# Kernel optimization log

Hardware: AMD Instinct MI355X
Metric: run time of the kernel (lower is better)

The kernel has to match this reference:

```python
import jax, jax.numpy as jnp
import numpy as np
from jax import lax

SCALES = [0.5, 0.25, 0.125, 0.0625]
D_MODEL = 256
IN_CH = 1


def setup_inputs() -> dict:
    key = jax.random.key(0)
    ks = jax.random.split(key, 16)
    x = jax.random.normal(ks[0], (2, D_MODEL, 256, 256), dtype=jnp.float32)
    m = jax.random.uniform(ks[1], (2, IN_CH, 256, 256), dtype=jnp.float32)
    s = 0.05
    Wq = jax.random.normal(ks[2], (D_MODEL, D_MODEL, 1, 1), jnp.float32) * s
    bq = jax.random.normal(ks[3], (D_MODEL,), jnp.float32) * s
    Wk = jax.random.normal(ks[4], (D_MODEL, D_MODEL, 1, 1), jnp.float32) * s
    bk = jax.random.normal(ks[5], (D_MODEL,), jnp.float32) * s
    Wv = jax.random.normal(ks[6], (D_MODEL, D_MODEL, 1, 1), jnp.float32) * s
    bv = jax.random.normal(ks[7], (D_MODEL,), jnp.float32) * s
    Wmq = jax.random.normal(ks[8], (D_MODEL, IN_CH, 1, 1), jnp.float32) * s
    bmq = jax.random.normal(ks[9], (D_MODEL,), jnp.float32) * s
    Wmk = jax.random.normal(ks[10], (D_MODEL, IN_CH, 1, 1), jnp.float32) * s
    bmk = jax.random.normal(ks[11], (D_MODEL,), jnp.float32) * s
    Wo = jax.random.normal(ks[12], (D_MODEL, D_MODEL, 3, 3), jnp.float32) * s
    bo = jax.random.normal(ks[13], (D_MODEL,), jnp.float32) * s
    return {"x": x, "m": m, "Wq": Wq, "bq": bq, "Wk": Wk, "bk": bk,
            "Wv": Wv, "bv": bv, "Wmq": Wmq, "bmq": bmq, "Wmk": Wmk, "bmk": bmk,
            "Wo": Wo, "bo": bo, "b": 1, "c": 256}


def _conv1x1(z, W, bias):
    # W: (O, I, 1, 1)
    return jnp.einsum('bihw,oi->bohw', z, W[:, :, 0, 0]) + bias[None, :, None, None]


def _forward(x, m, Wq, bq, Wk, bk, Wv, bv, Wmq, bmq, Wmk, bmk, Wo, bo, b, c):
    bt, _, h, w = x.shape  # h, w are multiples of 64 -> pad is zero
    t = bt // b
    n_scales = len(SCALES)
    d_k = c // n_scales

    q = _conv1x1(x, Wq, bq)
    k = _conv1x1(x, Wk, bk)
    v = _conv1x1(x, Wv, bv)
    mq = _conv1x1(m, Wmq, bmq)
    mk = _conv1x1(m, Wmk, bmk)

    outs = []
    for i, scale in enumerate(SCALES):
        height, width = int(h * scale), int(w * scale)
        out_h, out_w = h // height, w // width
        sl = slice(i * d_k, (i + 1) * d_k)

        def patch(z):
            # (b, t, d_k, out_h, height, out_w, width) -> (b, t*out_h*out_w, d_k*height*width)
            z = z[:, sl].reshape(b, t, d_k, out_h, height, out_w, width)
            z = z.transpose(0, 1, 3, 5, 2, 4, 6)
            return z.reshape(b, t * out_h * out_w, d_k * height * width)

        Q, K, V = patch(q), patch(k), patch(v)
        MQ, MK = patch(mq), patch(mk)
        inv_sqrt_d = 1.0 / jnp.sqrt(jnp.asarray(Q.shape[-1], jnp.float32))
        scores = jnp.einsum('bnd,bmd->bnm', Q, K) * inv_sqrt_d
        mask_scores = jnp.einsum('bnd,bmd->bnm', MQ, MK) * inv_sqrt_d
        p_attn = jax.nn.softmax(scores * mask_scores, axis=-1)
        y = jnp.einsum('bnm,bmd->bnd', p_attn, V)
        # back to (bt, d_k, h, w)
        y = y.reshape(b, t, out_h, out_w, d_k, height, width)
        y = y.transpose(0, 1, 4, 2, 5, 3, 6).reshape(bt, d_k, h, w)
        outs.append(y)

    out = jnp.concatenate(outs, axis=1)
    z = lax.conv_general_dilated(out, Wo, window_strides=(1, 1),
                                 padding=((1, 1), (1, 1)),
                                 dimension_numbers=('NCHW', 'OIHW', 'NCHW'))
    z = z + bo[None, :, None, None]
    return jnp.where(z > 0, z, 0.2 * z)  # LeakyReLU(0.2)


def reference(x, m, Wq, bq, Wk, bk, Wv, bv, Wmq, bmq, Wmk, bmk, Wo, bo, b, c):
    return _forward(x, m, Wq, bq, Wk, bk, Wv, bv, Wmq, bmq, Wmk, bmk, Wo, bo, b, c)
```

## Files before the change

kernel.cpp:

```cpp
#include <hip/hip_runtime.h>
#include <stdint.h>


typedef __attribute__((ext_vector_type(8))) short short8;
typedef __attribute__((ext_vector_type(4))) float floatx4;
typedef __attribute__((ext_vector_type(4))) unsigned int uintx4;

#define DEV static __device__ __forceinline__

DEV unsigned short f2bf(float f) {
  unsigned u = __builtin_bit_cast(unsigned, f);
  unsigned r = u + 0x7FFFu + ((u >> 16) & 1u);
  return (unsigned short)(r >> 16);
}

DEV void patch_row(int n, int sc, int lw, int& pt, int& sp0) {
  pt = n >> (2 + 2 * sc);
  int rem = n & ((4 << (2 * sc)) - 1);
  int oh = rem >> (1 + sc), ow = rem & ((2 << sc) - 1);
  sp0 = (oh << (lw + 8)) + (ow << lw);
}

__global__ void k_prep(const float* __restrict__ Wq, const float* __restrict__ Wk,
                       const float* __restrict__ Wv, const float* __restrict__ bq,
                       const float* __restrict__ bk, const float* __restrict__ bv,
                       const float* __restrict__ Wmq, const float* __restrict__ bmq,
                       const float* __restrict__ Wmk, const float* __restrict__ bmk,
                       const float* __restrict__ Wo, const float* __restrict__ bo,
                       unsigned short* __restrict__ wqkv, float* __restrict__ bias,
                       float* __restrict__ msc, unsigned short* __restrict__ wobf,
                       float* __restrict__ scoresG, unsigned int* __restrict__ pbuf) {
  int bid = blockIdx.x;
  int t = threadIdx.x;
  if (bid < 768) {
    const float* src = bid < 256 ? (Wq + bid * 256) : (bid < 512 ? (Wk + (bid - 256) * 256)
                                                                 : (Wv + (bid - 512) * 256));
    wqkv[bid * 256 + t] = f2bf(src[t]);
    if (t == 0) bias[bid] = bid < 256 ? bq[bid] : (bid < 512 ? bk[bid - 256] : bv[bid - 512]);
    return;
  }
  if (bid == 768) {
    int sc = t >> 6, lane = t & 63;
    int ch = sc * 64 + lane;
    float a0 = Wmq[ch] * Wmk[ch];
    float a1 = Wmq[ch] * bmk[ch];
    float a2 = bmq[ch] * Wmk[ch];
    float a3 = bmq[ch] * bmk[ch];
    for (int off = 32; off; off >>= 1) {
      a0 += __shfl_xor(a0, off); a1 += __shfl_xor(a1, off);
      a2 += __shfl_xor(a2, off); a3 += __shfl_xor(a3, off);
    }
    if (lane == 0) {
      msc[sc * 4 + 0] = a0; msc[sc * 4 + 1] = a1;
      msc[sc * 4 + 2] = a2; msc[sc * 4 + 3] = a3;
    }
    return;
  }
  int blk = bid - 769;
  if (blk < 2304) {
    int didx = blk >> 8, o = blk & 255, c = t;
    wobf[didx * 65536 + o * 256 + c] = f2bf(Wo[o * 2304 + c * 9 + didx]);
  } else {
    int i = (blk - 2304) * 256 + t;
    if (i < 559232) scoresG[i] = 0.f;
    if (i < 140032) pbuf[i] = 0u;
  }
}

__global__ __launch_bounds__(256) void k_xt(const float* __restrict__ x,
                                            unsigned short* __restrict__ xt) {
  __shared__ __align__(16) unsigned short tile[64][72];
  int p0 = blockIdx.x * 64, c0 = blockIdx.y * 64, t = blockIdx.z;
  int tid = threadIdx.x;
  {
    int cc = tid >> 2, pq = (tid & 3) * 16;
    const float* src = x + ((t * 256 + c0 + cc) * 65536 + p0 + pq);
    __align__(16) unsigned short tmp[16];
#pragma unroll
    for (int e = 0; e < 16; e += 4) {
      floatx4 v = *(const floatx4*)(src + e);
      tmp[e + 0] = f2bf(v[0]); tmp[e + 1] = f2bf(v[1]);
      tmp[e + 2] = f2bf(v[2]); tmp[e + 3] = f2bf(v[3]);
    }
    *(uintx4*)&tile[cc][pq] = *(const uintx4*)&tmp[0];
    *(uintx4*)&tile[cc][pq + 8] = *(const uintx4*)&tmp[8];
  }
  __syncthreads();
  {
    int pp = tid >> 2, cg = (tid & 3) * 16;
    __align__(16) unsigned short outv[16];
#pragma unroll
    for (int e = 0; e < 16; ++e) outv[e] = tile[cg + e][pp];
    unsigned short* dst = xt + ((t * 65536 + p0 + pp) * 256 + c0 + cg);
    *(uintx4*)dst = *(const uintx4*)&outv[0];
    *(uintx4*)(dst + 8) = *(const uintx4*)&outv[8];
  }
}

__global__ __launch_bounds__(256) void k_yt(const unsigned short* __restrict__ ynat,
                                            unsigned short* __restrict__ yt) {
  __shared__ __align__(16) unsigned short tile[64][72];
  int p0 = blockIdx.x * 64, c0 = blockIdx.y * 64, t = blockIdx.z;
  int tid = threadIdx.x;
  {
    int cc = tid >> 2, pq = (tid & 3) * 16;
    const unsigned short* src = ynat + ((t * 256 + c0 + cc) * 65536 + p0 + pq);
    *(uintx4*)&tile[cc][pq] = *(const uintx4*)src;
    *(uintx4*)&tile[cc][pq + 8] = *(const uintx4*)(src + 8);
  }
  __syncthreads();
  {
    int pp = tid >> 2, cg = (tid & 3) * 16;
    __align__(16) unsigned short outv[16];
#pragma unroll
    for (int e = 0; e < 16; ++e) outv[e] = tile[cg + e][pp];
    unsigned short* dst = yt + ((t * 65536 + p0 + pp) * 256 + c0 + cg);
    *(uintx4*)dst = *(const uintx4*)&outv[0];
    *(uintx4*)(dst + 8) = *(const uintx4*)&outv[8];
  }
}

__global__ __launch_bounds__(256, 2) void k_qkv(const unsigned short* __restrict__ xt,
                                                const unsigned short* __restrict__ wqkv,
                                                const float* __restrict__ bias,
                                                unsigned short* __restrict__ qkv) {
  extern __shared__ __align__(16) char smem[];
  auto As = (unsigned short (*)[64])(smem);
  auto Bs = (unsigned short (*)[64])(smem + 16384);
  auto Cs = (unsigned short (*)[280])(smem);
  int flat = blockIdx.x;
  int lg = (flat & 7) * 384 + (flat >> 3);
  int n_t = lg / 6, m_t = lg - n_t * 6;
  int n0 = n_t << 8, m0 = m_t << 7;
  int tid = threadIdx.x;
  int w = tid >> 6, l = tid & 63;
  int wr = w >> 1, wc = w & 1;
  int l15 = l & 15, lhi = l >> 4;
  int sr = tid >> 1, sbase = (tid & 1) * 4, r7 = sr & 7;
  int b7 = tid & 7;
  const unsigned short* gA = wqkv + (m0 + sr) * 256 + sbase * 8;
  const unsigned short* gB = xt + (n0 + tid) * 256;
  floatx4 zf = {0.f, 0.f, 0.f, 0.f};
  floatx4 acc[4][8];
#pragma unroll
  for (int i = 0; i < 4; ++i)
#pragma unroll
    for (int j = 0; j < 8; ++j) acc[i][j] = zf;
  uintx4 ra[4], rb[8];
#define QLOAD(K0) { const uintx4* pa = (const uintx4*)(gA + (K0)); \
                    ra[0] = pa[0]; ra[1] = pa[1]; ra[2] = pa[2]; ra[3] = pa[3]; \
                    const uintx4* pb = (const uintx4*)(gB + (K0)); \
                    rb[0] = pb[0]; rb[1] = pb[1]; rb[2] = pb[2]; rb[3] = pb[3]; \
                    rb[4] = pb[4]; rb[5] = pb[5]; rb[6] = pb[6]; rb[7] = pb[7]; }
  QLOAD(0);
#pragma unroll
  for (int ch = 0; ch < 4; ++ch) {
    __syncthreads();
#pragma unroll
    for (int j = 0; j < 4; ++j)
      *(uintx4*)&As[sr][((sbase + j) ^ r7) * 8] = ra[j];
#pragma unroll
    for (int j = 0; j < 8; ++j)
      *(uintx4*)&Bs[tid][(j ^ b7) * 8] = rb[j];
    __syncthreads();
    if (ch < 3) QLOAD((ch + 1) * 64);
#pragma unroll
    for (int kk = 0; kk < 2; ++kk) {
      short8 af[4];
#pragma unroll
      for (int f = 0; f < 4; ++f) {
        int arow = wr * 64 + f * 16 + l15;
        af[f] = *(const short8*)&As[arow][(((kk << 2) + lhi) ^ (arow & 7)) * 8];
      }
#pragma unroll
      for (int fn = 0; fn < 8; ++fn) {
        int brow = wc * 128 + fn * 16 + l15;
        short8 b = *(const short8*)&Bs[brow][(((kk << 2) + lhi) ^ (brow & 7)) * 8];
#pragma unroll
        for (int fm = 0; fm < 4; ++fm)
          acc[fm][fn] = __builtin_amdgcn_mfma_f32_16x16x32_bf16(af[fm], b, acc[fm][fn], 0, 0, 0);
      }
    }
  }
#undef QLOAD
#pragma unroll
  for (int h = 0; h < 2; ++h) {
    __syncthreads();
    if (wr == h) {
#pragma unroll
      for (int fm = 0; fm < 4; ++fm) {
#pragma unroll
        for (int rr = 0; rr < 4; ++rr) {
          int rl = fm * 16 + lhi * 4 + rr;
          float bv = bias[m0 + h * 64 + rl];
#pragma unroll
          for (int fn = 0; fn < 8; ++fn)
            Cs[rl][wc * 128 + fn * 16 + l15] = f2bf(acc[fm][fn][rr] + bv);
        }
      }
    }
    __syncthreads();
    {
      int p8 = (tid & 31) * 8;
      int pcol = n0 + p8;
      int t = pcol >> 16, p = pcol & 65535;
#pragma unroll
      for (int pass = 0; pass < 8; ++pass) {
        int rl = (tid >> 5) + pass * 8;
        uintx4 v = *(const uintx4*)&Cs[rl][p8];
        *(uintx4*)&qkv[((t * 768 + m0 + h * 64 + rl) << 16) + p] = v;
      }
    }
  }
}

__global__ __launch_bounds__(256) void k_mask(const float* __restrict__ m,
                                              float* __restrict__ G,
                                              float* __restrict__ rbuf) {
  int bid = blockIdx.x;
  int tid = threadIdx.x;
  if (bid >= 328) {
    int row = (bid - 328) * 4 + (tid >> 6);
    int lane = tid & 63;
    if (row < 680) {
      int sc, n;
      if (row < 8)        { sc = 0; n = row; }
      else if (row < 40)  { sc = 1; n = row - 8; }
      else if (row < 168) { sc = 2; n = row - 40; }
      else                { sc = 3; n = row - 168; }
      int lw = 7 - sc, W = 1 << lw;
      int pt, sp0;
      patch_row(n, sc, lw, pt, sp0);
      int base = pt * 65536 + sp0;
      int S = 1 << (14 - 2 * sc);
      float acc = 0.f;
      for (int s = lane; s < S; s += 64) {
        int hh = s >> lw, ww = s & (W - 1);
        acc += m[base + (hh << 8) + ww];
      }
      for (int off = 32; off; off >>= 1) acc += __shfl_xor(acc, off);
      if (lane == 0) rbuf[row] = acc;
    }
    return;
  }
  __shared__ __align__(16) float Ns[32][68];
  __shared__ __align__(16) float Ms[32][68];
  int sc, tn, tm, z, nchunks, soff;
  if (bid < 32)      { sc = 0; tn = 0; tm = 0; z = bid;      nchunks = 8; soff = 0; }
  else if (bid < 40) { sc = 1; tn = 0; tm = 0; z = bid - 32; nchunks = 8; soff = 64; }
  else if (bid < 72) { int r = bid - 40; int tl = r >> 1; sc = 2; tn = tl >> 2; tm = tl & 3; z = r & 1; nchunks = 8; soff = 1088; }
  else               { int tl = bid - 72; sc = 3; tn = tl >> 4; tm = tl & 15; z = 0; nchunks = 4; soff = 17472; }
  int lw = 7 - sc, W = 1 << lw, N = 8 << (2 * sc);
  int kbase = z * nchunks * 64;
  int n0 = tn * 32, m0 = tm * 32;
  bool isA = tid < 128;
  int u = tid & 127;
  int srow = u >> 2, sslot0 = (u & 3) * 4;
  int grow = (isA ? n0 : m0) + srow;
  bool valid = grow < N;
  int pt = 0, sp0 = 0;
  if (valid) patch_row(grow, sc, lw, pt, sp0);
  int gbase = pt * 65536 + sp0;
  int trc = tid >> 4, tcc = tid & 15;
  float a00 = 0.f, a01 = 0.f, a10 = 0.f, a11 = 0.f;
  floatx4 zf = {0.f, 0.f, 0.f, 0.f};
  for (int c = 0; c < nchunks; ++c) {
    int k0 = kbase + c * 64;
    floatx4 v[4];
#pragma unroll
    for (int j = 0; j < 4; ++j) {
      v[j] = zf;
      if (valid) {
        int s = k0 + (sslot0 + j) * 4;
        int hh = s >> lw, ww = s & (W - 1);
        v[j] = *(const floatx4*)(m + gbase + (hh << 8) + ww);
      }
    }
    __syncthreads();
    float* dstrow = isA ? &Ns[srow][0] : &Ms[srow][0];
#pragma unroll
    for (int j = 0; j < 4; ++j) *(floatx4*)&dstrow[(sslot0 + j) * 4] = v[j];
    __syncthreads();
#pragma unroll 4
    for (int k = 0; k < 64; k += 4) {
      floatx4 na = *(const floatx4*)&Ns[2 * trc][k];
      floatx4 nb = *(const floatx4*)&Ns[2 * trc + 1][k];
      floatx4 ma = *(const floatx4*)&Ms[2 * tcc][k];
      floatx4 mb = *(const floatx4*)&Ms[2 * tcc + 1][k];
#pragma unroll
      for (int e = 0; e < 4; ++e) {
        a00 += na[e] * ma[e]; a01 += na[e] * mb[e];
        a10 += nb[e] * ma[e]; a11 += nb[e] * mb[e];
      }
    }
  }
  int rn = n0 + 2 * trc, rm = m0 + 2 * tcc;
  float res[2][2] = {{a00, a01}, {a10, a11}};
#pragma unroll
  for (int i = 0; i < 2; ++i)
#pragma unroll
    for (int j = 0; j < 2; ++j) {
      if (rn + i < N && rm + j < N) {
        float* dst = &G[soff + (rn + i) * N + rm + j];
        if (sc < 3) atomicAdd(dst, res[i][j]); else *dst = res[i][j];
      }
    }
}

__global__ __launch_bounds__(256) void k_scores_all(const unsigned short* __restrict__ qkv,
                                                    float* __restrict__ scores) {
  __shared__ __align__(16) char sbuf[32768];
  int bid = blockIdx.x;
  int tid = threadIdx.x;
  int w = tid >> 6, l = tid & 63;
  int wr = w >> 1, wc = w & 1, l15 = l & 15, lhi = l >> 4;
  uintx4 zu = {0u, 0u, 0u, 0u};
  floatx4 zf = {0.f, 0.f, 0.f, 0.f};
  if (bid < 160) {
    auto As = (unsigned short (*)[64])(sbuf);
    auto Bs = (unsigned short (*)[64])(sbuf + 16384);
    int lg = (bid & 7) * 20 + (bid >> 3);
    int sc, tn, tm, z, soff;
    if (lg < 32) { sc = 2; tn = 0; tm = 0; z = lg; soff = 1088; }
    else { int r = lg - 32; int tl = r >> 3; sc = 3; tn = tl >> 2; tm = tl & 3; z = r & 7; soff = 17472; }
    int N = 8 << (2 * sc);
    int lw = 7 - sc, W = 1 << lw, lS = 14 - 2 * sc;
    int n0 = tn * 128, m0 = tm * 128;
    int kbase = z * 2048;
    int sr = tid >> 1, sbase = (tid & 1) * 4, r7 = sr & 7;
    int ptA, spA, ptB, spB;
    patch_row(n0 + sr, sc, lw, ptA, spA);
    patch_row(m0 + sr, sc, lw, ptB, spB);
    int baseA = (ptA * 768 + sc * 64) * 65536 + spA;
    int baseB = (ptB * 768 + 256 + sc * 64) * 65536 + spB;
    floatx4 acc[4][4];
#pragma unroll
    for (int i = 0; i < 4; ++i)
#pragma unroll
      for (int j = 0; j < 4; ++j) acc[i][j] = zf;
    uintx4 ra[4], rb[4];
#define GLOAD(K0) { \
  _Pragma("unroll") for (int j = 0; j < 4; ++j) { \
    int k = kbase + (K0) + (sbase + j) * 8; \
    int cl = k >> lS; int s = k & ((1 << lS) - 1); \
    int hh = s >> lw, ww = s & (W - 1); \
    int off = cl * 65536 + (hh << 8) + ww; \
    ra[j] = *(const uintx4*)(qkv + baseA + off); \
    rb[j] = *(const uintx4*)(qkv + baseB + off); } }
    GLOAD(0);
    for (int st = 0; st < 32; ++st) {
      __syncthreads();
#pragma unroll
      for (int j = 0; j < 4; ++j) {
        *(uintx4*)&As[sr][((sbase + j) ^ r7) * 8] = ra[j];
        *(uintx4*)&Bs[sr][((sbase + j) ^ r7) * 8] = rb[j];
      }
      __syncthreads();
      if (st < 31) GLOAD((st + 1) * 64);
#pragma unroll
      for (int kk = 0; kk < 2; ++kk) {
        short8 af[4], bfr[4];
#pragma unroll
        for (int f = 0; f < 4; ++f) {
          int arow = wr * 64 + f * 16 + l15;
          af[f] = *(const short8*)&As[arow][(((kk << 2) + lhi) ^ (arow & 7)) * 8];
          int brow = wc * 64 + f * 16 + l15;
          bfr[f] = *(const short8*)&Bs[brow][(((kk << 2) + lhi) ^ (brow & 7)) * 8];
        }
#pragma unroll
        for (int fm = 0; fm < 4; ++fm)
#pragma unroll
          for (int fn = 0; fn < 4; ++fn)
            acc[fm][fn] = __builtin_amdgcn_mfma_f32_16x16x32_bf16(af[fm], bfr[fn], acc[fm][fn], 0, 0, 0);
      }
    }
#undef GLOAD
#pragma unroll
    for (int fm = 0; fm < 4; ++fm) {
      int nrow = n0 + wr * 64 + fm * 16 + lhi * 4;
#pragma unroll
      for (int rr = 0; rr < 4; ++rr) {
#pragma unroll
        for (int fn = 0; fn < 4; ++fn) {
          int mcol = m0 + wc * 64 + fn * 16 + l15;
          atomicAdd(&scores[soff + (nrow + rr) * N + mcol], acc[fm][fn][rr]);
        }
      }
    }
    return;
  }
  {
    auto As = (unsigned short (*)[136])(sbuf);
    auto Bs = (unsigned short (*)[136])(sbuf + 8704);
    int b2 = bid - 160;
    int sc, z, soff;
    if (b2 < 256) { sc = 0; z = b2;       soff = 0; }
    else          { sc = 1; z = b2 - 256; soff = 64; }
    int lw = 7 - sc, W = 1 << lw, lS = 14 - 2 * sc, N = 8 << (2 * sc);
    int kbase = z * 4096;
    floatx4 acc = zf;
    bool isA = tid < 128;
    int u = tid & 127;
    int srow = u >> 2, sslot0 = (u & 3) * 4;
    int grow = srow;
    int cb = (isA ? 0 : 256) + sc * 64;
    int pt = 0, sp0 = 0;
    bool valid = grow < N;
    if (valid) patch_row(grow, sc, lw, pt, sp0);
    int rowbase = (pt * 768 + cb) * 65536 + sp0;
    uintx4 r[4];
#define SLOAD(KS) { int kb2 = kbase + (KS) * 128; \
  _Pragma("unroll") for (int j = 0; j < 4; ++j) { \
    uintx4 v = zu; \
    if (valid) { int k = kb2 + (sslot0 + j) * 8; \
      int cl = k >> lS; int s = k & ((1 << lS) - 1); \
      int hh = s >> lw, ww = s & (W - 1); \
      v = *(const uintx4*)(qkv + rowbase + cl * 65536 + (hh << 8) + ww); } \
    r[j] = v; } }
    SLOAD(0);
    for (int ks = 0; ks < 32; ++ks) {
      __syncthreads();
      {
        unsigned short* dstrow = isA ? &As[srow][0] : &Bs[srow][0];
#pragma unroll
        for (int j = 0; j < 4; ++j) *(uintx4*)&dstrow[(sslot0 + j) * 8] = r[j];
      }
      __syncthreads();
      if (ks < 31) SLOAD(ks + 1);
#pragma unroll
      for (int kk = 0; kk < 4; ++kk) {
        short8 a = *(const short8*)&As[wr * 16 + l15][(kk * 4 + lhi) * 8];
        short8 b = *(const short8*)&Bs[wc * 16 + l15][(kk * 4 + lhi) * 8];
        acc = __builtin_amdgcn_mfma_f32_16x16x32_bf16(a, b, acc, 0, 0, 0);
      }
    }
#undef SLOAD
    int rrow = wr * 16 + lhi * 4;
    int ccol = wc * 16 + l15;
    if (ccol < N) {
#pragma unroll
      for (int rr = 0; rr < 4; ++rr)
        if (rrow + rr < N) atomicAdd(&scores[soff + (rrow + rr) * N + ccol], acc[rr]);
    }
  }
}

__global__ void k_softmax(const float* __restrict__ scores, const float* __restrict__ G,
                          const float* __restrict__ rbuf, const float* __restrict__ msc,
                          unsigned short* __restrict__ pbuf) {
  int row = blockIdx.x, lane = threadIdx.x;
  int sc, n, roff, soff, poff;
  if (row < 8)        { sc = 0; n = row;       roff = 0;   soff = 0;     poff = 0; }
  else if (row < 40)  { sc = 1; n = row - 8;   roff = 8;   soff = 64;    poff = 512; }
  else if (row < 168) { sc = 2; n = row - 40;  roff = 40;  soff = 1088;  poff = 1536; }
  else                { sc = 3; n = row - 168; roff = 168; soff = 17472; poff = 17920; }
  int N = 8 << (2 * sc);
  int Kpad = (sc < 2) ? 32 : N;
  float Sf = (float)(1 << (14 - 2 * sc));
  float invD = 1.0f / (float)(1 << (20 - 2 * sc));
  float alpha = msc[sc * 4 + 0], beta = msc[sc * 4 + 1];
  float gamma = msc[sc * 4 + 2], delta = msc[sc * 4 + 3];
  float rn = rbuf[roff + n];
  float vals[8];
  float mx = -1e30f;
#pragma unroll
  for (int j = 0; j < 8; ++j) {
    float v = -1e30f;
    int mcol = lane + j * 64;
    if (j * 64 < N && mcol < N) {
      float sq = scores[soff + n * N + mcol];
      float g = G[soff + n * N + mcol];
      float rm = rbuf[roff + mcol];
      v = sq * (alpha * g + beta * rn + gamma * rm + delta * Sf) * invD;
    }
    vals[j] = v;
    mx = fmaxf(mx, v);
  }
  for (int off = 32; off; off >>= 1) mx = fmaxf(mx, __shfl_xor(mx, off));
  float sum = 0.f;
#pragma unroll
  for (int j = 0; j < 8; ++j) {
    int mcol = lane + j * 64;
    float e = 0.f;
    if (j * 64 < N && mcol < N) e = __expf(vals[j] - mx);
    vals[j] = e;
    sum += e;
  }
  for (int off = 32; off; off >>= 1) sum += __shfl_xor(sum, off);
  float inv = 1.f / sum;
#pragma unroll
  for (int j = 0; j < 8; ++j) {
    int mcol = lane + j * 64;
    if (j * 64 < N && mcol < N) pbuf[poff + n * Kpad + mcol] = f2bf(vals[j] * inv);
  }
}

__global__ __launch_bounds__(256) void k_pv(const unsigned short* __restrict__ qkv,
                                            const unsigned short* __restrict__ pbuf,
                                            unsigned short* __restrict__ ynat) {
  int bid = blockIdx.x;
  int sc, bx, by;
  if (bid < 4096)      { sc = 0; bx = bid; by = 0; }
  else if (bid < 6144) { sc = 1; bx = bid - 4096; by = 0; }
  else if (bid < 8192) { int r = bid - 6144; sc = 2; bx = r >> 1; by = r & 1; }
  else                 { int r = bid - 8192; sc = 3; bx = r >> 3; by = r & 7; }
  int WR    = (sc == 0) ? 1 : (sc == 1) ? 2 : 4;
  int logWC = (sc == 0) ? 2 : (sc == 1) ? 1 : 0;
  int poff  = (sc == 0) ? 0 : (sc == 1) ? 512 : (sc == 2) ? 1536 : 17920;
  int lw = 7 - sc, W = 1 << lw;
  int lS = 14 - 2 * sc;
  int N = 8 << (2 * sc);
  int Kpad = (sc < 2) ? 32 : N;
  int WC = 1 << logWC;
  int d0 = bx * (WC * 64);
  int nb = by * (WR * 16);
  __shared__ __align__(16) unsigned short As[2][64][40];
  __shared__ __align__(16) unsigned short Bt[2][256][32];
  int tid = threadIdx.x;
  int w = tid >> 6, l = tid & 63;
  int wr = w >> logWC, wc = w & (WC - 1);
  int l15 = l & 15, lhi = l >> 4;
  floatx4 zf = {0.f, 0.f, 0.f, 0.f};
  floatx4 acc[4];
#pragma unroll
  for (int i = 0; i < 4; ++i) acc[i] = zf;
  int bmp = tid & 15;
  int dg = tid >> 4;
  bool act0 = (WC > 1) || (dg < 8);
  bool has1 = (WC == 4);
  bool doA = tid < WR * 64;
  int arow = tid >> 2, akg = (tid & 3) * 8;
  int ksteps = Kpad >> 5;
  uintx4 zu = {0u, 0u, 0u, 0u};
  int vcb = (512 + sc * 64) * 65536;
  uintx4 av = zu, lo0 = zu, hi0 = zu, lo1 = zu, hi1 = zu;
#define PLOADS(KS) { int k0 = (KS) * 32; \
    av = zu; lo0 = zu; hi0 = zu; lo1 = zu; hi1 = zu; \
    if (doA) av = *(const uintx4*)(pbuf + poff + (nb + arow) * Kpad + k0 + akg); \
    int gm0 = k0 + 2 * bmp, gm1 = gm0 + 1; \
    bool mv0 = gm0 < N, mv1 = gm1 < N; \
    int pt0 = 0, sp00 = 0, pt1 = 0, sp01 = 0; \
    if (mv0) patch_row(gm0, sc, lw, pt0, sp00); \
    if (mv1) patch_row(gm1, sc, lw, pt1, sp01); \
    { int d = d0 + dg * 8; int cl = d >> lS; int s = d & ((1 << lS) - 1); \
      int hh = s >> lw, ww = s & (W - 1); int sp = (hh << 8) + ww; \
      if (act0 && mv0) lo0 = *(const uintx4*)(qkv + pt0 * 768 * 65536 + vcb + cl * 65536 + sp00 + sp); \
      if (act0 && mv1) hi0 = *(const uintx4*)(qkv + pt1 * 768 * 65536 + vcb + cl * 65536 + sp01 + sp); } \
    if (has1) { int d = d0 + (dg + 16) * 8; int cl = d >> lS; int s = d & ((1 << lS) - 1); \
      int hh = s >> lw, ww = s & (W - 1); int sp = (hh << 8) + ww; \
      if (mv0) lo1 = *(const uintx4*)(qkv + pt0 * 768 * 65536 + vcb + cl * 65536 + sp00 + sp); \
      if (mv1) hi1 = *(const uintx4*)(qkv + pt1 * 768 * 65536 + vcb + cl * 65536 + sp01 + sp); } }
  PLOADS(0);
  for (int ks = 0; ks < ksteps; ++ks) {
    int b = ks & 1;
    if (doA) *(uintx4*)&As[b][arow][akg] = av;
    if (act0) {
      int du = dg * 8;
#pragma unroll
      for (int j = 0; j < 8; ++j) {
        int d = du + j;
        unsigned losh = (lo0[j >> 1] >> ((j & 1) * 16)) & 0xFFFFu;
        unsigned hish = (hi0[j >> 1] >> ((j & 1) * 16)) & 0xFFFFu;
        unsigned wv = losh | (hish << 16);
        int slot = (bmp >> 2) ^ ((d >> 1) & 3) ^ ((d >> 3) & 3);
        ((unsigned int*)&Bt[b][d][0])[slot * 4 + (bmp & 3)] = wv;
      }
    }
    if (has1) {
      int du = (dg + 16) * 8;
#pragma unroll
      for (int j = 0; j < 8; ++j) {
        int d = du + j;
        unsigned losh = (lo1[j >> 1] >> ((j & 1) * 16)) & 0xFFFFu;
        unsigned hish = (hi1[j >> 1] >> ((j & 1) * 16)) & 0xFFFFu;
        unsigned wv = losh | (hish << 16);
        int slot = (bmp >> 2) ^ ((d >> 1) & 3) ^ ((d >> 3) & 3);
        ((unsigned int*)&Bt[b][d][0])[slot * 4 + (bmp & 3)] = wv;
      }
    }
    __syncthreads();
    if (ks + 1 < ksteps) PLOADS(ks + 1);
    short8 a = *(const short8*)&As[b][wr * 16 + l15][lhi * 8];
#pragma unroll
    for (int fn = 0; fn < 4; ++fn) {
      int row = wc * 64 + fn * 16 + l15;
      int slot = lhi ^ ((row >> 1) & 3) ^ ((row >> 3) & 3);
      short8 bb = *(const short8*)&Bt[b][row][slot * 8];
      acc[fn] = __builtin_amdgcn_mfma_f32_16x16x32_bf16(a, bb, acc[fn], 0, 0, 0);
    }
  }
#undef PLOADS
  int nrow = nb + wr * 16 + lhi * 4;
#pragma unroll
  for (int rr = 0; rr < 4; ++rr) {
    int n = nrow + rr;
    if (n < N) {
      int pt, sp0;
      patch_row(n, sc, lw, pt, sp0);
#pragma unroll
      for (int fn = 0; fn < 4; ++fn) {
        int d = d0 + wc * 64 + fn * 16 + l15;
        int cl = d >> lS;
        int s = d & ((1 << lS) - 1);
        int hh = s >> lw, ww = s & (W - 1);
        int c = sc * 64 + cl;
        ynat[(pt * 256 + c) * 65536 + sp0 + (hh << 8) + ww] = f2bf(acc[fn][rr]);
      }
    }
  }
}

__global__ __launch_bounds__(256, 3) void k_conv(const unsigned short* __restrict__ yt,
                                                 const unsigned short* __restrict__ wo,
                                                 const float* __restrict__ bo,
                                                 float* __restrict__ out) {
  __shared__ __align__(16) unsigned short As[64][128];
  __shared__ __align__(16) unsigned short Bs[130][64];
  int flat = blockIdx.x;
  int lg = ((flat & 7) << 8) + (flat >> 3);
  int n_t = lg >> 2, m_t = lg & 3;
  int n0 = n_t << 8, m0 = m_t << 6;
  int tt = n0 >> 16, yy = (n0 >> 8) & 255;
  int tid = threadIdx.x;
  int w = tid >> 6, l = tid & 63;
  int l15 = l & 15, lhi = l >> 4;
  bool doA = tid < 192;
  int a_dx = tid >> 6, a_o = tid & 63;
  bool doBh = tid >= 254;
  floatx4 zf = {0.f, 0.f, 0.f, 0.f};
  floatx4 acc[4][4];
#pragma unroll
  for (int i = 0; i < 4; ++i)
#pragma unroll
    for (int j = 0; j < 4; ++j) acc[i][j] = zf;
  uintx4 zu = {0u, 0u, 0u, 0u};
  uintx4 rb[4], ra[4], rh[4];
  const unsigned short* ybase = yt + (tt << 24);
#define CLOAD(ST) { \
    int dy = (ST) >> 3, cc = ((ST) & 7) << 5; \
    int yq = yy + dy - 1; \
    bool yv = (unsigned)yq < 256u; \
    { int xq = tid - 1; \
      if (yv && (unsigned)xq < 256u) { \
        const uintx4* p = (const uintx4*)(ybase + ((yq << 8) + xq) * 256 + cc); \
        rb[0] = p[0]; rb[1] = p[1]; rb[2] = p[2]; rb[3] = p[3]; \
      } else { rb[0] = zu; rb[1] = zu; rb[2] = zu; rb[3] = zu; } } \
    if (doA) { \
      const uintx4* p = (const uintx4*)(wo + (dy * 3 + a_dx) * 65536 + (m0 + a_o) * 256 + cc); \
      ra[0] = p[0]; ra[1] = p[1]; ra[2] = p[2]; ra[3] = p[3]; \
    } else if (doBh) { \
      int xq = tid + 1;   \
      if (yv && xq < 256) { \
        const uintx4* p = (const uintx4*)(ybase + ((yq << 8) + xq) * 256 + cc); \
        rh[0] = p[0]; rh[1] = p[1]; rh[2] = p[2]; rh[3] = p[3]; \
      } else { rh[0] = zu; rh[1] = zu; rh[2] = zu; rh[3] = zu; } } }
  CLOAD(0);
  for (int st = 0; st < 24; ++st) {
    __syncthreads();
    {
      int brow = tid >> 1, bhf = (tid & 1) * 4, br7 = brow & 7;
#pragma unroll
      for (int j = 0; j < 4; ++j)
        *(uintx4*)&Bs[brow][((bhf + j) ^ br7) * 8] = rb[j];
      if (doA) {
        int o7 = a_o & 7;
#pragma unroll
        for (int j = 0; j < 4; ++j)
          *(uintx4*)&As[a_o][((a_dx * 4 + j) ^ o7) * 8] = ra[j];
      } else if (doBh) {
        int xh = tid + 2;
        int brow2 = xh >> 1, bhf2 = (xh & 1) * 4, br72 = brow2 & 7;
#pragma unroll
        for (int j = 0; j < 4; ++j)
          *(uintx4*)&Bs[brow2][((bhf2 + j) ^ br72) * 8] = rh[j];
      }
    }
    __syncthreads();
    if (st < 23) CLOAD(st + 1);
#pragma unroll
    for (int dx = 0; dx < 3; ++dx) {
      short8 af[4];
#pragma unroll
      for (int f = 0; f < 4; ++f) {
        int ol = f * 16 + l15;
        af[f] = *(const short8*)&As[ol][((dx * 4 + lhi) ^ (ol & 7)) * 8];
      }
#pragma unroll
      for (int fn = 0; fn < 4; ++fn) {
        int xh = w * 64 + fn * 16 + l15 + dx;
        short8 b = *(const short8*)&Bs[xh >> 1][((((xh & 1) * 4 + lhi)) ^ ((xh >> 1) & 7)) * 8];
#pragma unroll
        for (int fm = 0; fm < 4; ++fm)
          acc[fm][fn] = __builtin_amdgcn_mfma_f32_16x16x32_bf16(af[fm], b, acc[fm][fn], 0, 0, 0);
      }
    }
  }
#undef CLOAD
#pragma unroll
  for (int fm = 0; fm < 4; ++fm) {
    int o = m0 + fm * 16 + lhi * 4;
#pragma unroll
    for (int rr = 0; rr < 4; ++rr) {
      float bias = bo[o + rr];
#pragma unroll
      for (int fn = 0; fn < 4; ++fn) {
        int xcol = w * 64 + fn * 16 + l15;
        float z = acc[fm][fn][rr] + bias;
        out[((tt * 256 + o + rr) << 16) + (yy << 8) + xcol] = z > 0.f ? z : 0.2f * z;
      }
    }
  }
}

extern "C" void kernel_launch(void* const* d_in, const int* in_sizes, int n_in,
                              void* d_out, int out_size, void* d_ws, size_t ws_size,
                              hipStream_t stream) {
  const float* x   = (const float*)d_in[0];
  const float* m   = (const float*)d_in[1];
  const float* Wq  = (const float*)d_in[2];
  const float* bq  = (const float*)d_in[3];
  const float* Wk  = (const float*)d_in[4];
  const float* bk  = (const float*)d_in[5];
  const float* Wv  = (const float*)d_in[6];
  const float* bv  = (const float*)d_in[7];
  const float* Wmq = (const float*)d_in[8];
  const float* bmq = (const float*)d_in[9];
  const float* Wmk = (const float*)d_in[10];
  const float* bmk = (const float*)d_in[11];
  const float* Wo  = (const float*)d_in[12];
  const float* bo  = (const float*)d_in[13];

  char* ws = (char*)d_ws;
  unsigned short* qkv   = (unsigned short*)(ws);
  unsigned short* xtb   = (unsigned short*)(ws + 201326592);
  unsigned short* wqkv  = (unsigned short*)(ws + 268435456);
  unsigned short* wobf  = (unsigned short*)(ws + 268828672);
  float* bias           = (float*)(ws + 270008320);
  float* msc            = (float*)(ws + 270011392);
  float* scores         = (float*)(ws + 270011456);
  float* G              = (float*)(ws + 271129920);
  float* rbuf           = (float*)(ws + 272248384);
  unsigned short* pbuf  = (unsigned short*)(ws + 272251104);
  float* out            = (float*)d_out;
  unsigned short* ynat  = (unsigned short*)d_out;

  k_prep<<<dim3(5258), dim3(256), 0, stream>>>(Wq, Wk, Wv, bq, bk, bv, Wmq, bmq, Wmk, bmk,
                                               Wo, bo, wqkv, bias, msc, wobf, scores,
                                               (unsigned int*)pbuf);
  k_xt<<<dim3(1024, 4, 2), dim3(256), 0, stream>>>(x, xtb);
  k_qkv<<<dim3(3072), dim3(256), 49152, stream>>>(xtb, wqkv, bias, qkv);
  k_mask<<<dim3(498), dim3(256), 0, stream>>>(m, G, rbuf);
  k_scores_all<<<dim3(480), dim3(256), 0, stream>>>(qkv, scores);
  k_softmax<<<dim3(680), dim3(64), 0, stream>>>(scores, G, rbuf, msc, pbuf);
  k_pv<<<dim3(10240), dim3(256), 0, stream>>>(qkv, pbuf, ynat);
  k_yt<<<dim3(1024, 4, 2), dim3(256), 0, stream>>>(ynat, xtb);
  k_conv<<<dim3(2048), dim3(256), 0, stream>>>(xtb, wobf, bo, out);
}
```

Measured before the change: 576.4 us.

## Enlarge conv output tile to 128x256 and remap k_pv block order for locality

The 3x3 conv kernel now computes 128 output channels per block instead of 64, with a 2x2 wave layout and 32 accumulators per lane. Each staged input row tile is therefore reused across twice as many output channels, and only half as many blocks are launched. In exchange, register use rises and occupancy drops from 3 to 2 blocks per CU, with larger LDS use. Separately, k_pv renumbers its blocks for scales 2 and 3 so that blocks running at the same time share data better in cache.

```diff
diff --git a/kernel.cpp b/kernel.cpp
--- a/kernel.cpp
+++ b/kernel.cpp
@@ -498,7 +498,17 @@
 __global__ __launch_bounds__(256) void k_pv(const unsigned short* __restrict__ qkv,
                                             const unsigned short* __restrict__ pbuf,
                                             unsigned short* __restrict__ ynat) {
-  int bid = blockIdx.x;
+  int bid0 = blockIdx.x;
+  int bid;
+  if (bid0 < 6144) {
+    bid = bid0;
+  } else if (bid0 < 8192) {
+    int q = bid0 - 6144; int c = q & 7, j = q >> 3;
+    bid = 6144 + ((c * 128 + (j & 127)) << 1) + (j >> 7);
+  } else {
+    int q = bid0 - 8192; int c = q & 7, j = q >> 3;
+    bid = 8192 + ((c * 32 + (j & 31)) << 3) + (j >> 5);
+  }
   int sc, bx, by;
   if (bid < 4096)      { sc = 0; bx = bid; by = 0; }
   else if (bid < 6144) { sc = 1; bx = bid - 4096; by = 0; }
@@ -610,31 +620,32 @@
   }
 }
 
-__global__ __launch_bounds__(256, 3) void k_conv(const unsigned short* __restrict__ yt,
+__global__ __launch_bounds__(256, 2) void k_conv(const unsigned short* __restrict__ yt,
                                                  const unsigned short* __restrict__ wo,
                                                  const float* __restrict__ bo,
                                                  float* __restrict__ out) {
-  __shared__ __align__(16) unsigned short As[64][128];
+  __shared__ __align__(16) unsigned short As[128][128];
   __shared__ __align__(16) unsigned short Bs[130][64];
   int flat = blockIdx.x;
-  int lg = ((flat & 7) << 8) + (flat >> 3);
-  int n_t = lg >> 2, m_t = lg & 3;
-  int n0 = n_t << 8, m0 = m_t << 6;
+  int lg = ((flat & 7) << 7) + (flat >> 3);
+  int n_t = lg >> 1, m_t = lg & 1;
+  int n0 = n_t << 8, m0 = m_t << 7;
   int tt = n0 >> 16, yy = (n0 >> 8) & 255;
   int tid = threadIdx.x;
   int w = tid >> 6, l = tid & 63;
+  int wr = w >> 1, wc = w & 1;
   int l15 = l & 15, lhi = l >> 4;
-  bool doA = tid < 192;
-  int a_dx = tid >> 6, a_o = tid & 63;
+  int a_d0 = tid >> 7, a_o0 = tid & 127;
+  bool doA1 = tid < 128;
   bool doBh = tid >= 254;
   floatx4 zf = {0.f, 0.f, 0.f, 0.f};
-  floatx4 acc[4][4];
+  floatx4 acc[4][8];
 #pragma unroll
   for (int i = 0; i < 4; ++i)
 #pragma unroll
-    for (int j = 0; j < 4; ++j) acc[i][j] = zf;
+    for (int j = 0; j < 8; ++j) acc[i][j] = zf;
   uintx4 zu = {0u, 0u, 0u, 0u};
-  uintx4 rb[4], ra[4], rh[4];
+  uintx4 rb[4], ra0[4], ra1[4];
   const unsigned short* ybase = yt + (tt << 24);
 #define CLOAD(ST) { \
     int dy = (ST) >> 3, cc = ((ST) & 7) << 5; \
@@ -645,15 +656,17 @@
         const uintx4* p = (const uintx4*)(ybase + ((yq << 8) + xq) * 256 + cc); \
         rb[0] = p[0]; rb[1] = p[1]; rb[2] = p[2]; rb[3] = p[3]; \
       } else { rb[0] = zu; rb[1] = zu; rb[2] = zu; rb[3] = zu; } } \
-    if (doA) { \
-      const uintx4* p = (const uintx4*)(wo + (dy * 3 + a_dx) * 65536 + (m0 + a_o) * 256 + cc); \
-      ra[0] = p[0]; ra[1] = p[1]; ra[2] = p[2]; ra[3] = p[3]; \
+    { const uintx4* p = (const uintx4*)(wo + (dy * 3 + a_d0) * 65536 + (m0 + a_o0) * 256 + cc); \
+      ra0[0] = p[0]; ra0[1] = p[1]; ra0[2] = p[2]; ra0[3] = p[3]; } \
+    if (doA1) { \
+      const uintx4* p = (const uintx4*)(wo + (dy * 3 + 2) * 65536 + (m0 + tid) * 256 + cc); \
+      ra1[0] = p[0]; ra1[1] = p[1]; ra1[2] = p[2]; ra1[3] = p[3]; \
     } else if (doBh) { \
-      int xq = tid + 1;   \
+      int xq = tid + 1; \
       if (yv && xq < 256) { \
         const uintx4* p = (const uintx4*)(ybase + ((yq << 8) + xq) * 256 + cc); \
-        rh[0] = p[0]; rh[1] = p[1]; rh[2] = p[2]; rh[3] = p[3]; \
-      } else { rh[0] = zu; rh[1] = zu; rh[2] = zu; rh[3] = zu; } } }
+        ra1[0] = p[0]; ra1[1] = p[1]; ra1[2] = p[2]; ra1[3] = p[3]; \
+      } else { ra1[0] = zu; ra1[1] = zu; ra1[2] = zu; ra1[3] = zu; } } }
   CLOAD(0);
   for (int st = 0; st < 24; ++st) {
     __syncthreads();
@@ -662,17 +675,21 @@
 #pragma unroll
       for (int j = 0; j < 4; ++j)
         *(uintx4*)&Bs[brow][((bhf + j) ^ br7) * 8] = rb[j];
-      if (doA) {
-        int o7 = a_o & 7;
+      int ao7 = a_o0 & 7;
+#pragma unroll
+      for (int j = 0; j < 4; ++j)
+        *(uintx4*)&As[a_o0][((a_d0 * 4 + j) ^ ao7) * 8] = ra0[j];
+      if (doA1) {
+        int o7 = tid & 7;
 #pragma unroll
         for (int j = 0; j < 4; ++j)
-          *(uintx4*)&As[a_o][((a_dx * 4 + j) ^ o7) * 8] = ra[j];
+          *(uintx4*)&As[tid][((8 + j) ^ o7) * 8] = ra1[j];
       } else if (doBh) {
         int xh = tid + 2;
         int brow2 = xh >> 1, bhf2 = (xh & 1) * 4, br72 = brow2 & 7;
 #pragma unroll
         for (int j = 0; j < 4; ++j)
-          *(uintx4*)&Bs[brow2][((bhf2 + j) ^ br72) * 8] = rh[j];
+          *(uintx4*)&Bs[brow2][((bhf2 + j) ^ br72) * 8] = ra1[j];
       }
     }
     __syncthreads();
@@ -682,12 +699,12 @@
       short8 af[4];
 #pragma unroll
       for (int f = 0; f < 4; ++f) {
-        int ol = f * 16 + l15;
+        int ol = wr * 64 + f * 16 + l15;
         af[f] = *(const short8*)&As[ol][((dx * 4 + lhi) ^ (ol & 7)) * 8];
       }
 #pragma unroll
-      for (int fn = 0; fn < 4; ++fn) {
-        int xh = w * 64 + fn * 16 + l15 + dx;
+      for (int fn = 0; fn < 8; ++fn) {
+        int xh = wc * 128 + fn * 16 + l15 + dx;
         short8 b = *(const short8*)&Bs[xh >> 1][((((xh & 1) * 4 + lhi)) ^ ((xh >> 1) & 7)) * 8];
 #pragma unroll
         for (int fm = 0; fm < 4; ++fm)
@@ -698,13 +715,13 @@
 #undef CLOAD
 #pragma unroll
   for (int fm = 0; fm < 4; ++fm) {
-    int o = m0 + fm * 16 + lhi * 4;
+    int o = m0 + wr * 64 + fm * 16 + lhi * 4;
 #pragma unroll
     for (int rr = 0; rr < 4; ++rr) {
       float bias = bo[o + rr];
 #pragma unroll
-      for (int fn = 0; fn < 4; ++fn) {
-        int xcol = w * 64 + fn * 16 + l15;
+      for (int fn = 0; fn < 8; ++fn) {
+        int xcol = wc * 128 + fn * 16 + l15;
         float z = acc[fm][fn][rr] + bias;
         out[((tt * 256 + o + rr) << 16) + (yy << 8) + xcol] = z > 0.f ? z : 0.2f * z;
       }
@@ -754,5 +771,5 @@
   k_softmax<<<dim3(680), dim3(64), 0, stream>>>(scores, G, rbuf, msc, pbuf);
   k_pv<<<dim3(10240), dim3(256), 0, stream>>>(qkv, pbuf, ynat);
   k_yt<<<dim3(1024, 4, 2), dim3(256), 0, stream>>>(ynat, xtb);
-  k_conv<<<dim3(2048), dim3(256), 0, stream>>>(xtb, wobf, bo, out);
-}
+  k_conv<<<dim3(1024), dim3(256), 0, stream>>>(xtb, wobf, bo, out);
+}
```

New measurement: 528.1 us. 8.4% less time.
